# Kernel optimization log

Measured on AMD Instinct MI355X. Metric: run time of the kernel, lower is better.

The kernel has to match this reference:

```python
import jax, jax.numpy as jnp
import numpy as np
from jax.scipy.linalg import cho_solve

B, T, N, L, R, H, S = 32, 256, 256, 64, 16, 256, 8


def mT(A):
    return jnp.swapaxes(A, -1, -2)


def bmv(A, x):
    return jnp.einsum('...ij,...j->...i', A, x)


def bip(x, y):
    return jnp.sum(x * y, axis=-1)


def chol_bmv_solve(chol, v):
    return cho_solve((chol, True), v[..., None])[..., 0]


def setup_inputs():
    key = jax.random.key(0)
    ks = jax.random.split(key, 8)
    y = 3.0 * jax.random.uniform(ks[0], (B, T, N), dtype=jnp.float32)  # nonneg 'counts'
    eps = jax.random.normal(ks[1], (S, B, T, L), dtype=jnp.float32)    # reparam noise
    W1 = jax.random.normal(ks[2], (N, H), dtype=jnp.float32) / np.float32(np.sqrt(N))
    b1 = jnp.zeros((H,), jnp.float32)
    W2 = 0.05 * jax.random.normal(ks[3], (H, L + L * R), dtype=jnp.float32)
    b2 = jnp.zeros((L + L * R,), jnp.float32)
    F = 0.9 * jnp.linalg.qr(jax.random.normal(ks[4], (L, L), dtype=jnp.float32))[0]  # stable dynamics
    log_Q = jnp.full((L,), -1.0, jnp.float32)
    log_Q_0 = jnp.zeros((L,), jnp.float32)
    m_0 = 0.1 * jax.random.normal(ks[5], (L,), dtype=jnp.float32)
    C = jax.random.normal(ks[6], (N, L), dtype=jnp.float32) / np.float32(np.sqrt(L))
    b_read = jnp.full((N,), -1.0, jnp.float32)
    return dict(y=y, eps=eps, W1=W1, b1=b1, W2=W2, b2=b2, F=F, log_Q=log_Q,
                log_Q_0=log_Q_0, m_0=m_0, C=C, b_read=b_read, n_samples=S)


def _kf_update(m_p, P_p, k_t, J_t):
    # information-form measurement update: J_f = P_p^{-1} + J_t
    I = jnp.eye(P_p.shape[-1], dtype=P_p.dtype)
    Pp_chol = jnp.linalg.cholesky(P_p)
    h_p = chol_bmv_solve(Pp_chol, m_p)
    J_p = cho_solve((Pp_chol, True), jnp.broadcast_to(I, P_p.shape))
    J_f = J_p + J_t
    Jf_chol = jnp.linalg.cholesky(0.5 * (J_f + mT(J_f)))
    P_f = cho_solve((Jf_chol, True), jnp.broadcast_to(I, J_f.shape))
    P_f = 0.5 * (P_f + mT(P_f))
    m_f = chol_bmv_solve(Jf_chol, h_p + k_t)
    return m_f, P_f


def kalman_information_filter(k, J, F, Q_diag, m_0, Q_0_diag):
    Bb, Tt, Ll = k.shape
    m_p0 = jnp.broadcast_to(m_0, (Bb, Ll))
    P_p0 = jnp.broadcast_to(jnp.diag(Q_0_diag), (Bb, Ll, Ll))
    m_f0, P_f0 = _kf_update(m_p0, P_p0, k[:, 0], J[:, 0])
    Qd = jnp.diag(Q_diag)

    def step(carry, inp):
        m_prev, P_prev = carry
        k_t, J_t = inp
        m_p = m_prev @ F.T
        P_p = F @ P_prev @ F.T + Qd
        m_f, P_f = _kf_update(m_p, P_p, k_t, J_t)
        return (m_f, P_f), (m_f, P_f, m_p, P_p)

    inp = (jnp.swapaxes(k[:, 1:], 0, 1), jnp.swapaxes(J[:, 1:], 0, 1))
    _, (m_f_r, P_f_r, m_p_r, P_p_r) = jax.lax.scan(step, (m_f0, P_f0), inp)
    cat = lambda x0, xr: jnp.concatenate([x0[:, None], jnp.swapaxes(xr, 0, 1)], axis=1)
    return cat(m_f0, m_f_r), cat(P_f0, P_f_r), cat(m_p0, m_p_r), cat(P_p0, P_p_r)


def rts_smoother(m_p, P_p, m_f, P_f, F):
    def step(carry, inp):
        m_s_n, P_s_n = carry
        m_f_t, P_f_t, m_p_n, P_p_n = inp
        Pp_chol = jnp.linalg.cholesky(P_p_n)
        G = mT(cho_solve((Pp_chol, True), F @ P_f_t))  # G = P_f F^T P_p^{-1}
        m_s = m_f_t + bmv(G, m_s_n - m_p_n)
        P_s = P_f_t + G @ (P_s_n - P_p_n) @ mT(G)
        P_s = 0.5 * (P_s + mT(P_s))
        return (m_s, P_s), (m_s, P_s)

    inp = (jnp.swapaxes(m_f[:, :-1], 0, 1), jnp.swapaxes(P_f[:, :-1], 0, 1),
           jnp.swapaxes(m_p[:, 1:], 0, 1), jnp.swapaxes(P_p[:, 1:], 0, 1))
    _, (m_s_r, P_s_r) = jax.lax.scan(step, (m_f[:, -1], P_f[:, -1]), inp, reverse=True)
    m = jnp.concatenate([jnp.swapaxes(m_s_r, 0, 1), m_f[:, -1:]], axis=1)
    P = jnp.concatenate([jnp.swapaxes(P_s_r, 0, 1), P_f[:, -1:]], axis=1)
    return m, P


def alt_kl_step_0(m_s, m_f, m_0, P_s, Q_0_diag, a, A):
    P_sA = P_s @ A
    P_pA = A * Q_0_diag[:, None]
    AmTP_sA = mT(A) @ P_sA
    AmTP_pA = mT(A) @ P_pA
    AmTm_s = bmv(mT(A), m_s)
    AmTm_f = bmv(mT(A), m_f)
    P_p_inv_m_f = m_f / Q_0_diag
    P_p_inv_m_p = m_0 / Q_0_diag
    Ir = jnp.eye(A.shape[-1], dtype=A.dtype)
    logdet_triple = jnp.linalg.slogdet(Ir + AmTP_pA)[1]
    inner_p = bip(a, m_s) - 0.5 * bip(AmTm_s, AmTm_s) - 0.5 * jnp.trace(AmTP_sA, axis1=-2, axis2=-1)
    delta_logZ = 0.5 * (bip(m_f, P_p_inv_m_f) - bip(m_0, P_p_inv_m_p) + bip(AmTm_f, AmTm_f) - logdet_triple)
    return inner_p - delta_logZ


def alt_kl_step_t(m_s, m_f, m_p, P_s, P_p, a, A):
    P_sA = P_s @ A
    P_pA = P_p @ A
    P_p_chol = jnp.linalg.cholesky(P_p)
    AmTP_sA = mT(A) @ P_sA
    AmTP_pA = mT(A) @ P_pA
    AmTm_s = bmv(mT(A), m_s)
    AmTm_f = bmv(mT(A), m_f)
    P_p_inv_m_f = chol_bmv_solve(P_p_chol, m_f)
    P_p_inv_m_p = chol_bmv_solve(P_p_chol, m_p)
    Ir = jnp.eye(A.shape[-1], dtype=A.dtype)
    logdet_triple = jnp.linalg.slogdet(Ir + AmTP_pA)[1]
    inner_p = bip(a, m_s) - 0.5 * bip(AmTm_s, AmTm_s) - 0.5 * jnp.trace(AmTP_sA, axis1=-2, axis2=-1)
    delta_logZ = 0.5 * (bip(m_f, P_p_inv_m_f) - bip(m_p, P_p_inv_m_p) + bip(AmTm_f, AmTm_f) - logdet_triple)
    return inner_p - delta_logZ


def _forward(y, eps, W1, b1, W2, b2, F, log_Q, log_Q_0, m_0, C, b_read):
    # local encoder (all masks are identity since p_mask_* = 0)
    h = jnp.tanh(y @ W1 + b1)
    out = h @ W2 + b2
    k_y = out[..., :L]                                   # [B,T,L]
    K_y = out[..., L:].reshape(y.shape[0], y.shape[1], L, R)  # [B,T,L,R]
    Q_diag = jax.nn.softplus(log_Q)
    Q_0_diag = jax.nn.softplus(log_Q_0)
    m_f, P_f, m_p, P_p = kalman_information_filter(k_y, K_y @ mT(K_y), F, Q_diag, m_0, Q_0_diag)
    m, P = rts_smoother(m_p, P_p, m_f, P_f, F)
    kl_1 = alt_kl_step_0(m[:, 0], m_f[:, 0], m_0, P[:, 0], Q_0_diag, k_y[:, 0], K_y[:, 0])
    kl_t = alt_kl_step_t(m[:, 1:], m_f[:, 1:], m_p[:, 1:], P[:, 1:], P_p[:, 1:], k_y[:, 1:], K_y[:, 1:])
    kl = jnp.concatenate([kl_1[:, None], kl_t], axis=1)  # [B,T]
    P_chol = jnp.linalg.cholesky(P + 1e-5 * jnp.eye(L, dtype=P.dtype))
    z_s = m + bmv(P_chol, eps)                            # [S,B,T,L]
    log_rate = jnp.einsum('sbtl,nl->sbtn', z_s, C) + b_read
    ell = jnp.sum(y * log_rate - jnp.exp(log_rate), axis=-1).mean(axis=0)  # [B,T]
    return jnp.mean(jnp.sum(kl - ell, axis=-1))


def reference(y, eps, W1, b1, W2, b2, F, log_Q, log_Q_0, m_0, C, b_read, n_samples):
    return _forward(y, eps, W1, b1, W2, b2, F, log_Q, log_Q_0, m_0, C, b_read)
```

## Files before the change

kernel.cpp:

```cpp
#include <hip/hip_runtime.h>
#include <math.h>

#define B_ 32
#define T_ 256
#define N_ 256
#define L_ 64
#define R_ 16
#define H_ 256
#define NS_ 8
#define SEG 32
#define NSEG 8
#define ST 65
#define STM 67
#define STF 68
#define SBF 72
#define SU 20
#define PKN 2080
#define PIDX(i,j) ((((i)*((i)+1))>>1) + (j))

using f32x4  = __attribute__((ext_vector_type(4))) float;
using bf16x8 = __attribute__((ext_vector_type(8))) short;
using s16x4  = __attribute__((ext_vector_type(4))) short;

__device__ __forceinline__ float softplus_f(float x) { return log1pf(expf(x)); }
// ... 20 lines not shown
{ return __uint_as_float(((unsigned)(unsigned short)s)<<16); }

template<int SB>
__device__ __forceinline__ void mfma_mm64(const short* Ah, const short* Al,
                                          const short* Bh, const short* Bl,
                                          int w, int l, f32x4 acc[4])
{
  const int lr = l & 15, lg = l >> 4;
  const int arow = (w*16+lr)*SB;
#pragma unroll
  for (int ks = 0; ks < 2; ++ks) {
    const int ko = ks*32 + lg*8;
    bf16x8 ah = *(const bf16x8*)&Ah[arow + ko];
    bf16x8 al = *(const bf16x8*)&Al[arow + ko];
#pragma unroll
    for (int ct = 0; ct < 4; ++ct) {
      bf16x8 bh = *(const bf16x8*)&Bh[(ct*16+lr)*SB + ko];
      bf16x8 bl = *(const bf16x8*)&Bl[(ct*16+lr)*SB + ko];
      acc[ct] = __builtin_amdgcn_mfma_f32_16x16x32_bf16(ah, bh, acc[ct], 0,0,0);
      acc[ct] = __builtin_amdgcn_mfma_f32_16x16x32_bf16(ah, bl, acc[ct], 0,0,0);
      acc[ct] = __builtin_amdgcn_mfma_f32_16x16x32_bf16(al, bh, acc[ct], 0,0,0);
    }
  }
}

template<int SA>
__device__ __forceinline__ void chol64_blk(float* A, float* rdiag, float* dg, int tid)
{
#pragma unroll
  for (int kb = 0; kb < 4; ++kb) {
    const int o = kb*16;
    if (tid < 16) {
      const int ln = tid;
      float s[16];
#pragma unroll
      for (int j = 0; j < 16; ++j) s[j] = A[(o+ln)*SA + o + j];
#pragma unroll
      for (int k = 0; k < 16; ++k) {
        const float dk = fmaxf(__shfl(s[k], k, 64), 1e-30f);
        const float d = sqrtf(dk);
        const float rd = 1.f/d;
        const float lik = s[k]*rd;
        if (ln == k) { rdiag[o+k] = rd; if (dg) dg[o+k] = d; }
#pragma unroll
        for (int j = 0; j < 16; ++j) {
          const float ljk = __shfl(lik, j, 64);
          if (j > k && j <= ln) s[j] -= lik*ljk;
        }
        if (ln > k) s[k] = lik;
        else if (ln == k) s[k] = dk;
      }
#pragma unroll
      for (int j = 0; j < 16; ++j) A[(o+ln)*SA + o + j] = s[j];
    }
    __syncthreads();
    const int nr = 48 - o;
    if (nr > 0) {
      if (tid < nr) {
        const int r = o + 16 + tid;
        float x[16];
#pragma unroll
        for (int q = 0; q < 16; ++q) x[q] = A[r*SA + o + q];
#pragma unroll
        for (int j = 0; j < 16; ++j) {
          x[j] *= rdiag[o+j];
#pragma unroll
          for (int i2 = j+1; i2 < 16; ++i2) x[i2] -= A[(o+i2)*SA + o + j] * x[j];
        }
#pragma unroll
        for (int q = 0; q < 16; ++q) A[r*SA + o + q] = x[q];
      }
      __syncthreads();
      const int tot = nr*nr;
      for (int idx = tid; idx < tot; idx += 256) {
        const int i = o + 16 + idx / nr, j = o + 16 + idx % nr;
        float acc = A[i*SA + j];
#pragma unroll
        for (int k = 0; k < 16; ++k) acc -= A[i*SA + o + k] * A[j*SA + o + k];
        A[i*SA + j] = acc;
      }
      __syncthreads();
    }
  }
}

__device__ __forceinline__ void fwd16(float* x, const float* sS, const float* sSd)
{
#pragma unroll
  for (int a = 0; a < 16; ++a) {
    x[a] *= sSd[a];
#pragma unroll
    for (int i = a+1; i < 16; ++i) x[i] -= sS[i*17+a]*x[a];
  }
}

template<bool TANH, bool SPLIT>
__global__ __launch_bounds__(256) void gemm_kernel(
    const float* __restrict__ A, const float* __restrict__ Bw,
    const float* __restrict__ bias, float* __restrict__ C1,
    float* __restrict__ C2, int M, int Nn, int Kk)
{
  __shared__ float As[16][65];
  __shared__ float Bs[16][64];
  const int bm = blockIdx.y * 64, bn = blockIdx.x * 64;
  const int tid = threadIdx.x;
  const int rg = tid >> 4, cg = tid & 15;
  float acc[4][4] = {{0.f}};
  for (int k0 = 0; k0 < Kk; k0 += 16) {
    {
      const int kk = tid & 15, r0 = tid >> 4;
#pragma unroll
      for (int rr = 0; rr < 4; ++rr)
        As[kk][r0 + 16*rr] = A[(size_t)(bm + r0 + 16*rr) * Kk + k0 + kk];
    }
    {
      const int cc = tid & 63, kk = tid >> 6;
#pragma unroll
      for (int kr = 0; kr < 4; ++kr)
        Bs[kk + 4*kr][cc] = Bw[(size_t)(k0 + kk + 4*kr) * Nn + bn + cc];
    }
    __syncthreads();
#pragma unroll
    for (int k = 0; k < 16; ++k) {
      float a[4], bb[4];
#pragma unroll
      for (int i = 0; i < 4; ++i) a[i] = As[k][rg*4+i];
#pragma unroll
      for (int j = 0; j < 4; ++j) bb[j] = Bs[k][cg*4+j];
#pragma unroll
      for (int i = 0; i < 4; ++i)
#pragma unroll
        for (int j = 0; j < 4; ++j) acc[i][j] += a[i]*bb[j];
    }
    __syncthreads();
  }
#pragma unroll
  for (int i = 0; i < 4; ++i) {
    const int row = bm + rg*4 + i;
#pragma unroll
    for (int j = 0; j < 4; ++j) {
      const int col = bn + cg*4 + j;
      float v = acc[i][j] + bias[col];
      if (TANH) v = tanhf(v);
      if (SPLIT) {
        if (col < 64) C1[(size_t)row*64 + col] = v;
        else          C2[(size_t)row*1024 + (col-64)] = v;
      } else {
        C1[(size_t)row*Nn + col] = v;
      }
    }
  }
}

__global__ __launch_bounds__(256, 1) void filter_kernel(
    const float* __restrict__ kyg, const float* __restrict__ Kxg,
    const float* __restrict__ Fg, const float* __restrict__ logQ,
    const float* __restrict__ logQ0, const float* __restrict__ m0g,
    float* __restrict__ mf_g, float* __restrict__ mp_g,
    float* __restrict__ Pf_g, float* __restrict__ dpart_g,
    float* __restrict__ mfT_g)
{
  __shared__ float sB[64*STF];
  __shared__ __align__(16) char sPool[18432];
  __shared__ short sFh[64*SBF], sFl[64*SBF];
  __shared__ float sS[16*17], sSd[16];
  __shared__ float sQ[64], sQ0[64], skv[64], smf[64], smp[64], sv[16], sw[16];
  __shared__ float sldv;
  __shared__ f32x4 sRed4[256];
  float* sRed = (float*)sRed4;
  short* sXh = (short*)sPool;
  short* sXl = (short*)(sPool + 9216);
  float* sU  = (float*)sPool;
  float* sK  = (float*)(sPool + 5120);

  const int b = blockIdx.x, tid = threadIdx.x;
  const int w = tid >> 6, l = tid & 63;

#pragma unroll
  for (int q = 0; q < 4; ++q) {
    const int idx = q*1024 + tid*4;
    const int row = idx>>6, col = idx&63;
    float4 v = *(const float4*)&Fg[idx];
    s16x4 h4, l4;
    splitbf4(v, h4, l4);
    *(s16x4*)&sFh[row*SBF+col] = h4;
    *(s16x4*)&sFl[row*SBF+col] = l4;
  }
  if (tid < 64) {
    sQ[tid]  = softplus_f(logQ[tid]);
    sQ0[tid] = softplus_f(logQ0[tid]);
    smf[tid] = m0g[tid];
  }
  __syncthreads();

  for (int t = 0; t < T_; ++t) {
    const size_t bt = (size_t)b*T_ + t;
    if (t == 0) {
      for (int i = tid; i < 4096; i += 256) {
        const int r = i>>6, c = i&63;
        sB[r*STF+c] = (r==c) ? sQ0[r] : 0.f;
      }
      const float4 kreg = ((const float4*)(Kxg + bt*1024))[tid];
      *(float4*)&sK[(tid>>2)*SU + (tid&3)*4] = kreg;
      if (tid < 64) { smp[tid] = smf[tid]; skv[tid] = kyg[bt*64 + tid]; mp_g[bt*64+tid] = smp[tid]; }
      __syncthreads();
    } else {
#pragma unroll
      for (int q = 0; q < 4; ++q) {
        const int idx = q*1024 + tid*4;
        const int row = idx>>6, col = idx&63;
        float4 v = *(const float4*)&sB[row*STF+col];
        s16x4 h4, l4;
        splitbf4(v, h4, l4);
        *(s16x4*)&sXh[row*SBF+col] = h4;
        *(s16x4*)&sXl[row*SBF+col] = l4;
      }
      __syncthreads();
      const float4 kreg = ((const float4*)(Kxg + bt*1024))[tid];
      float kvreg = 0.f;
      if (tid < 64) kvreg = kyg[bt*64 + tid];
      f32x4 acc[4];
#pragma unroll
      for (int ct = 0; ct < 4; ++ct) acc[ct] = (f32x4){0.f,0.f,0.f,0.f};
      mfma_mm64<SBF>(sFh, sFl, sXh, sXl, w, l, acc);
      {
        const int i = tid & 63, jb = tid >> 6;
        float s = 0.f;
#pragma unroll
        for (int hq = 0; hq < 2; ++hq) {
          bf16x8 fh = *(const bf16x8*)&sFh[i*SBF + jb*16 + hq*8];
          bf16x8 fl = *(const bf16x8*)&sFl[i*SBF + jb*16 + hq*8];
#pragma unroll
          for (int j = 0; j < 8; ++j)
            s += (bf2f(fh[j]) + bf2f(fl[j])) * smf[jb*16 + hq*8 + j];
        }
        sRed[tid] = s;
      }
      __syncthreads();
      {
        const int lr = l & 15, lg = l >> 4;
#pragma unroll
        for (int ct = 0; ct < 4; ++ct)
#pragma unroll
          for (int r = 0; r < 4; ++r) {
            short hh, ll;
            splitbf(acc[ct][r], hh, ll);
            const int row = w*16 + lg*4 + r, col = ct*16 + lr;
            sXh[row*SBF+col] = hh; sXl[row*SBF+col] = ll;
          }
      }
      if (tid < 64) {
        const float mpv = sRed[tid] + sRed[tid+64] + sRed[tid+128] + sRed[tid+192];
        smp[tid] = mpv; mp_g[bt*64+tid] = mpv;
      }
      __syncthreads();
#pragma unroll
      for (int ct = 0; ct < 4; ++ct) acc[ct] = (f32x4){0.f,0.f,0.f,0.f};
      mfma_mm64<SBF>(sXh, sXl, sFh, sFl, w, l, acc);
      __syncthreads();
      {
        const int lr = l & 15, lg = l >> 4;
#pragma unroll
        for (int ct = 0; ct < 4; ++ct)
#pragma unroll
          for (int r = 0; r < 4; ++r) {
            const int row = w*16 + lg*4 + r, col = ct*16 + lr;
            sB[row*STF+col] = acc[ct][r] + ((row==col) ? sQ[row] : 0.f);
          }
      }
      *(float4*)&sK[(tid>>2)*SU + (tid&3)*4] = kreg;
      if (tid < 64) skv[tid] = kvreg;
      __syncthreads();
    }
    {
      const int i = tid & 63, rq = tid >> 6;
      float4 u = {0.f,0.f,0.f,0.f};
      for (int jb = 0; jb < 16; ++jb) {
        const float4 p4 = *(const float4*)&sB[i*STF + jb*4];
#pragma unroll
        for (int dj = 0; dj < 4; ++dj) {
          const float4 k4 = *(const float4*)&sK[(jb*4+dj)*SU + rq*4];
          const float pv = (dj==0) ? p4.x : (dj==1) ? p4.y : (dj==2) ? p4.z : p4.w;
          u.x += pv*k4.x; u.y += pv*k4.y; u.z += pv*k4.z; u.w += pv*k4.w;
        }
      }
      *(float4*)&sU[i*SU + rq*4] = u;
    }
    __syncthreads();
    {
      const int ib = tid >> 6, r1 = (tid >> 2) & 15, r2b = tid & 3;
      float4 part = {0.f,0.f,0.f,0.f};
      for (int ii = 0; ii < 16; ++ii) {
        const int i = ib*16 + ii;
        const float kv = sK[i*SU + r1];
        const float4 u4 = *(const float4*)&sU[i*SU + r2b*4];
        part.x += kv*u4.x; part.y += kv*u4.y; part.z += kv*u4.z; part.w += kv*u4.w;
      }
      sRed4[tid] = (f32x4){part.x, part.y, part.z, part.w};
    }
    __syncthreads();
    if (tid < 64) {
      const int r1 = tid >> 2, r2b = tid & 3;
      f32x4 s4 = sRed4[tid];
      s4 += sRed4[tid+64]; s4 += sRed4[tid+128]; s4 += sRed4[tid+192];
#pragma unroll
      for (int dj = 0; dj < 4; ++dj)
        sS[r1*17 + r2b*4 + dj] = s4[dj] + ((r1 == r2b*4+dj) ? 1.f : 0.f);
    }
    __syncthreads();
    if (tid < 16) {
      const int ln = tid;
      float s[16];
#pragma unroll
      for (int j = 0; j < 16; ++j) s[j] = sS[ln*17+j];
      float pd = 1.f;
#pragma unroll
      for (int k = 0; k < 16; ++k) {
        const float dk = fmaxf(__shfl(s[k], k, 64), 1e-30f);
        const float d = sqrtf(dk);
        const float rd = 1.f/d;
        pd *= dk;
        const float lik = s[k]*rd;
        if (ln == k) sSd[k] = rd;
#pragma unroll
        for (int j = 0; j < 16; ++j) {
          const float ljk = __shfl(lik, j, 64);
          if (j > k && j <= ln) s[j] -= lik*ljk;
        }
        if (ln > k) s[k] = lik;
        else if (ln == k) s[k] = d;
      }
#pragma unroll
      for (int j = 0; j < 16; ++j) sS[ln*17+j] = s[j];
      if (ln == 0) sldv = logf(pd);
    } else if (tid >= 64 && tid < 80) {
      const int r = tid - 64;
      float a = 0.f;
      for (int i = 0; i < 64; ++i) a += sK[i*SU+r] * smp[i];
      sv[r] = a;
    }
    __syncthreads();
    if (tid < 64) {
      float x[16];
#pragma unroll
      for (int q = 0; q < 4; ++q) {
        const float4 u4 = *(const float4*)&sU[tid*SU + q*4];
        x[q*4+0]=u4.x; x[q*4+1]=u4.y; x[q*4+2]=u4.z; x[q*4+3]=u4.w;
      }
      fwd16(x, sS, sSd);
#pragma unroll
      for (int q = 0; q < 4; ++q) {
        float4 u4 = {x[q*4+0], x[q*4+1], x[q*4+2], x[q*4+3]};
        *(float4*)&sU[tid*SU + q*4] = u4;
      }
    } else if (tid == 64) {
      float x[16];
#pragma unroll
      for (int r = 0; r < 16; ++r) x[r] = sv[r];
      fwd16(x, sS, sSd);
#pragma unroll
      for (int r = 0; r < 16; ++r) sw[r] = x[r];
    }
    __syncthreads();
    {
      const int rg = tid >> 4, cg = tid & 15;
      float acc2[4][4] = {{0.f}};
#pragma unroll
      for (int rb = 0; rb < 4; ++rb) {
        float4 a4[4], b4[4];
#pragma unroll
        for (int i = 0; i < 4; ++i) a4[i] = *(const float4*)&sU[(rg*4+i)*SU + rb*4];
#pragma unroll
        for (int jj = 0; jj < 4; ++jj) b4[jj] = *(const float4*)&sU[(cg+16*jj)*SU + rb*4];
#pragma unroll
        for (int i = 0; i < 4; ++i)
#pragma unroll
          for (int jj = 0; jj < 4; ++jj)
            acc2[i][jj] += a4[i].x*b4[jj].x + a4[i].y*b4[jj].y
                         + a4[i].z*b4[jj].z + a4[i].w*b4[jj].w;
      }
#pragma unroll
      for (int i = 0; i < 4; ++i)
#pragma unroll
        for (int jj = 0; jj < 4; ++jj) {
          const int r = rg*4+i, c = cg+16*jj;
          sB[r*STF+c] -= acc2[i][jj];
        }
    }
    __syncthreads();
    {
      const int i = tid & 63, jb = tid >> 6;
      float s = 0.f;
#pragma unroll
      for (int q = 0; q < 4; ++q) {
        const float4 p4 = *(const float4*)&sB[i*STF + jb*16 + q*4];
        s += p4.x*skv[jb*16+q*4+0] + p4.y*skv[jb*16+q*4+1]
           + p4.z*skv[jb*16+q*4+2] + p4.w*skv[jb*16+q*4+3];
      }
      sRed[tid] = s;
    }
    for (int i2 = tid; i2 < 4096; i2 += 256)
      Pf_g[bt*4096+i2] = sB[(i2>>6)*STF+(i2&63)];
    __syncthreads();
    if (tid < 64) {
      float a = smp[tid];
#pragma unroll
      for (int q = 0; q < 4; ++q) {
        const float4 u4 = *(const float4*)&sU[tid*SU + q*4];
        a -= u4.x*sw[q*4+0] + u4.y*sw[q*4+1] + u4.z*sw[q*4+2] + u4.w*sw[q*4+3];
      }
      a += sRed[tid] + sRed[tid+64] + sRed[tid+128] + sRed[tid+192];
      smf[tid] = a;
      mf_g[bt*64+tid] = a;
      if (t == T_-1) mfT_g[b*64+tid] = a;
    }
    __syncthreads();
    if (tid < 16) {
      float a = 0.f;
      for (int i = 0; i < 64; ++i) a += sK[i*SU+tid]*smf[i];
      float aa = a*a;
      aa += __shfl_xor(aa, 1, 64);
      aa += __shfl_xor(aa, 2, 64);
      aa += __shfl_xor(aa, 4, 64);
      aa += __shfl_xor(aa, 8, 64);
      if (tid == 0) {
        float dp = aa - sldv;
        if (t == 0) {
          float d1 = 0.f, d2 = 0.f;
          for (int i = 0; i < 64; ++i) {
            d1 += smf[i]*smf[i]/sQ0[i];
            d2 += smp[i]*smp[i]/sQ0[i];
          }
          dp = 0.5f*(d1 - d2 + dp);
        }
        dpart_g[bt] = dp;
      }
    }
    __syncthreads();
  }
}

__global__ __launch_bounds__(256) void gains_kernel(
    const float* __restrict__ Fg, const float* __restrict__ logQ,
    const float* __restrict__ mf_g, const float* __restrict__ mp_g,
    float* __restrict__ PfG_g, float* __restrict__ Cpk,
    float* __restrict__ d_g, float* __restrict__ dpart_g)
{
  const int blk = blockIdx.x;
  const int b = blk / (T_-1);
  const int n = 1 + (blk % (T_-1));
  const size_t btn = (size_t)b*T_ + n;
  const size_t btm = btn - 1;
  const int tid = threadIdx.x;
  const int rg = tid >> 4, cg = tid & 15;
  __shared__ float sA[64*ST];
  __shared__ float sM[64*STM];
  __shared__ float sPp[64*ST];
  __shared__ float sDi[64], sQd[64];
  __shared__ float smf1[64], smp[64];
  __shared__ float sd1d2[2];

  for (int i = tid; i < 4096; i += 256) sA[(i>>6)*ST + (i&63)] = PfG_g[btm*4096+i];
  if (tid < 64) {
    sM[tid*STM+64] = mf_g[btn*64+tid];
    sM[tid*STM+65] = mp_g[btn*64+tid];
    smf1[tid] = mf_g[btm*64+tid];
    smp[tid]  = mp_g[btn*64+tid];
    sQd[tid]  = softplus_f(logQ[tid]);
  }
  __syncthreads();
  {
    float acc[4][4] = {{0.f}};
#pragma unroll 4
    for (int k = 0; k < 64; ++k) {
      float a[4], bb[4];
#pragma unroll
      for (int i = 0; i < 4; ++i) a[i] = Fg[(rg*4+i)*64 + k];
#pragma unroll
      for (int j = 0; j < 4; ++j) bb[j] = sA[k*ST + cg*4+j];
#pragma unroll
      for (int i = 0; i < 4; ++i)
#pragma unroll
        for (int j = 0; j < 4; ++j) acc[i][j] += a[i]*bb[j];
    }
#pragma unroll
    for (int i = 0; i < 4; ++i)
#pragma unroll
      for (int j = 0; j < 4; ++j) sM[(rg*4+i)*STM + cg*4+j] = acc[i][j];
  }
  __syncthreads();
  {
    float acc[4][4] = {{0.f}};
#pragma unroll 4
    for (int k = 0; k < 64; ++k) {
      float a[4], bb[4];
#pragma unroll
      for (int i = 0; i < 4; ++i) a[i] = sM[(rg*4+i)*STM + k];
#pragma unroll
      for (int j = 0; j < 4; ++j) bb[j] = Fg[(cg*4+j)*64 + k];
#pragma unroll
      for (int i = 0; i < 4; ++i)
#pragma unroll
        for (int j = 0; j < 4; ++j) acc[i][j] += a[i]*bb[j];
    }
#pragma unroll
    for (int i = 0; i < 4; ++i)
#pragma unroll
      for (int j = 0; j < 4; ++j) {
        const int r = rg*4+i, c = cg*4+j;
        sPp[r*ST+c] = acc[i][j] + ((r==c) ? sQd[r] : 0.f);
      }
  }
  __syncthreads();
  chol64_blk<ST>(sPp, sDi, (float*)nullptr, tid);
#pragma unroll
  for (int jb = 0; jb < 4; ++jb) {
    const int o = jb*16;
    if (tid < 66) {
      const int c = tid;
      float x[16];
#pragma unroll
      for (int q = 0; q < 16; ++q) x[q] = sM[(o+q)*STM + c];
#pragma unroll
      for (int j = 0; j < 16; ++j) {
        x[j] *= sDi[o+j];
#pragma unroll
        for (int i = j+1; i < 16; ++i) x[i] -= sPp[(o+i)*ST + o+j] * x[j];
      }
#pragma unroll
      for (int q = 0; q < 16; ++q) sM[(o+q)*STM + c] = x[q];
    }
    __syncthreads();
    const int nr = 48 - o;
    if (nr > 0) {
      for (int idx = tid; idx < nr*66; idx += 256) {
        const int r = o + 16 + idx/66, c = idx%66;
        float acc = sM[r*STM + c];
#pragma unroll
        for (int k = 0; k < 16; ++k) acc -= sPp[r*ST + o+k] * sM[(o+k)*STM + c];
        sM[r*STM + c] = acc;
      }
      __syncthreads();
    }
  }
  if (tid == 64 || tid == 65) {
    float a = 0.f;
    for (int i = 0; i < 64; ++i) { const float v = sM[i*STM+tid]; a += v*v; }
    sd1d2[tid-64] = a;
  }
  {
    float acc[4][4] = {{0.f}};
#pragma unroll 2
    for (int k = 0; k < 64; ++k) {
      float a[4], bb[4];
#pragma unroll
      for (int i = 0; i < 4; ++i) a[i] = sM[k*STM + rg*4+i];
#pragma unroll
      for (int j = 0; j < 4; ++j) bb[j] = sM[k*STM + cg*4+j];
#pragma unroll
      for (int i = 0; i < 4; ++i)
#pragma unroll
        for (int j = 0; j < 4; ++j) acc[i][j] += a[i]*bb[j];
    }
#pragma unroll
    for (int i = 0; i < 4; ++i)
#pragma unroll
      for (int j = 0; j < 4; ++j)
        sA[(rg*4+i)*ST + (cg*4+j)] -= acc[i][j];
  }
  __syncthreads();
  for (int idx = tid; idx < 4096; idx += 256) {
    const int i = idx>>6, j = idx&63;
// ... 434 lines not shown
  sy[tid]  = yg[bt*256+tid];
  sbr[tid] = brg[tid];
  for (int i = tid; i < NS_*64; i += 256) {
    const int s = i >> 6, j = i & 63;
    sE[i] = epsg[(((size_t)s*B_ + b)*T_ + t)*64 + j];
  }
  __syncthreads();
  {
    const int i = tid & 63, rq = tid >> 6;
    float u[4] = {0.f,0.f,0.f,0.f};
    for (int j = 0; j < 64; ++j) {
      const float p = sPs[i*ST+j];
#pragma unroll
      for (int r = 0; r < 4; ++r) u[r] += p * sK[j*17 + rq*4 + r];
    }
#pragma unroll
    for (int r = 0; r < 4; ++r) sPA[i*17 + rq*4 + r] = u[r];
  }
  __syncthreads();
  {
    const int i = tid & 63, rq = tid >> 6;
    float a = 0.f;
#pragma unroll
    for (int r = 0; r < 4; ++r) a += sK[i*17+rq*4+r]*sPA[i*17+rq*4+r];
    red[tid] = a;
  }
  if (tid < 16) {
    float a = 0.f;
    for (int i = 0; i < 64; ++i) a += sK[i*17+tid]*sms[i];
    sv[tid] = a;
  }
  __syncthreads();
  for (int s2 = 128; s2 > 0; s2 >>= 1) {
    if (tid < s2) red[tid] += red[tid+s2];
    __syncthreads();
  }
  float klv = 0.f;
  if (tid == 0) {
    const float tr = red[0];
    float ip1 = 0.f;
    for (int i = 0; i < 64; ++i) ip1 += skv[i]*sms[i];
    float s2s = 0.f;
#pragma unroll
    for (int r = 0; r < 16; ++r) s2s += sv[r]*sv[r];
    klv = (ip1 - 0.5f*s2s - 0.5f*tr) - dpart_g[bt];
  }
  if (tid < 64) sPs[tid*ST+tid] += 1e-5f;
  __syncthreads();
  chol64_blk<ST>(sPs, sDi, sDg, tid);
#pragma unroll
  for (int p = 0; p < 2; ++p) {
    const int s = (tid >> 6) + 4*p, ll = tid & 63;
    float a = sms[ll];
    for (int j = 0; j < ll; ++j) a += sPs[ll*ST+j]*sE[s*64+j];
    a += sDg[ll]*sE[s*64+ll];
    sZ[s*ST+ll] = a;
  }
  __syncthreads();
  float accel = 0.f;
  for (int nc = 0; nc < 4; ++nc) {
    for (int i = tid; i < 4096; i += 256) sC[(i>>6)*ST+(i&63)] = Cg[nc*4096+i];
    __syncthreads();
#pragma unroll
    for (int p = 0; p < 2; ++p) {
      const int idx = p*256 + tid;
      const int s = idx >> 6, rn = idx & 63;
      const int nn2 = nc*64 + rn;
      float lr = sbr[nn2];
      for (int ll = 0; ll < 64; ++ll) lr += sZ[s*ST+ll]*sC[rn*ST+ll];
      accel += sy[nn2]*lr - expf(lr);
    }
    __syncthreads();
  }
  red[tid] = accel;
  __syncthreads();
  for (int s2 = 128; s2 > 0; s2 >>= 1) {
    if (tid < s2) red[tid] += red[tid+s2];
    __syncthreads();
  }
  if (tid == 0) val_g[bt] = klv - red[0]*(1.0f/NS_);
}

__global__ __launch_bounds__(256) void reduce_kernel(const float* __restrict__ val,
                                                     float* __restrict__ out)
{
  __shared__ float red[256];
  float acc = 0.f;
  for (int i = threadIdx.x; i < B_*T_; i += 256) acc += val[i];
  red[threadIdx.x] = acc;
  __syncthreads();
  for (int s2 = 128; s2 > 0; s2 >>= 1) {
    if (threadIdx.x < s2) red[threadIdx.x] += red[threadIdx.x+s2];
    __syncthreads();
  }
  if (threadIdx.x == 0) out[0] = red[0] / (float)B_;
}

__global__ void diag_kernel(float* out, float v)
{
  if (threadIdx.x == 0) out[0] = v;
}

extern "C" void kernel_launch(void* const* d_in, const int* in_sizes, int n_in,
                              void* d_out, int out_size, void* d_ws, size_t ws_size,
                              hipStream_t stream)
{
  const float* y    = (const float*)d_in[0];
  const float* eps  = (const float*)d_in[1];
  const float* W1   = (const float*)d_in[2];
  const float* b1   = (const float*)d_in[3];
  const float* W2   = (const float*)d_in[4];
  const float* b2   = (const float*)d_in[5];
  const float* F    = (const float*)d_in[6];
  const float* logQ = (const float*)d_in[7];
  const float* logQ0= (const float*)d_in[8];
  const float* m0   = (const float*)d_in[9];
  const float* C    = (const float*)d_in[10];
  const float* br   = (const float*)d_in[11];
  (void)in_sizes; (void)n_in; (void)out_size;

  char* ws = (char*)d_ws;
  float* out = (float*)d_out;

  auto al = [](size_t x){ return (x + 255) & ~(size_t)255; };
  size_t o = 0;
  float* ky    = (float*)(ws + o); o = al(o + (size_t)B_*T_*64*4);
  float* mf    = (float*)(ws + o); o = al(o + (size_t)B_*T_*64*4);
  float* mp    = (float*)(ws + o); o = al(o + (size_t)B_*T_*64*4);
  float* msb   = (float*)(ws + o); o = al(o + (size_t)B_*T_*64*4);
  float* dv    = (float*)(ws + o); o = al(o + (size_t)B_*T_*64*4);
  float* dpart = (float*)(ws + o); o = al(o + (size_t)B_*T_*4);
  float* val   = (float*)(ws + o); o = al(o + (size_t)B_*T_*4);
  float* Kx    = (float*)(ws + o); o = al(o + (size_t)B_*T_*1024*4);
  float* A1    = (float*)(ws + o); o = al(o + (size_t)B_*T_*4096*4);
  float* Cpk   = (float*)(ws + o); o = al(o + (size_t)B_*T_*PKN*4);
  float* Gseg  = (float*)(ws + o); o = al(o + (size_t)B_*NSEG*4096*4);
  float* cseg  = (float*)(ws + o); o = al(o + (size_t)B_*NSEG*PKN*4);
  float* dseg  = (float*)(ws + o); o = al(o + (size_t)B_*NSEG*64*4);
  float* InP   = (float*)(ws + o); o = al(o + (size_t)B_*NSEG*PKN*4);
  float* Inm   = (float*)(ws + o); o = al(o + (size_t)B_*NSEG*64*4);
  float* mfT   = (float*)(ws + o); o = al(o + (size_t)B_*64*4);
  float* h     = A1;

  if (ws_size < o) {
    diag_kernel<<<1, 64, 0, stream>>>(out, (float)((double)ws_size / 1048576.0));
    return;
  }

  dim3 blk(256);
  gemm_kernel<true,false><<<dim3(H_/64, (B_*T_)/64), blk, 0, stream>>>(
      y, W1, b1, h, (float*)nullptr, B_*T_, H_, N_);
  gemm_kernel<false,true><<<dim3((L_+L_*R_)/64, (B_*T_)/64), blk, 0, stream>>>(
      h, W2, b2, ky, Kx, B_*T_, L_+L_*R_, H_);
  filter_kernel<<<B_, blk, 0, stream>>>(ky, Kx, F, logQ, logQ0, m0,
                                        mf, mp, A1, dpart, mfT);
  gains_kernel<<<B_*(T_-1), blk, 0, stream>>>(F, logQ, mf, mp, A1, Cpk, dv, dpart);
  compose_kernel<<<B_*NSEG, blk, 65536 + 8320 + 1024 + 256 + 64, stream>>>(
      A1, Cpk, dv, Gseg, cseg, dseg);
  boundary_kernel<<<B_, blk, 0, stream>>>(A1, mfT, Gseg, cseg, dseg, InP, Inm);
  expand_kernel<<<B_*NSEG, blk, 0, stream>>>(A1, Cpk, dv, InP, Inm, msb);
  klell_kernel<<<B_*T_, blk, 0, stream>>>(y, eps, ky, Kx, C, br, Cpk, msb, dpart, val);
  reduce_kernel<<<1, blk, 0, stream>>>(val, (float*)d_out);
}
```

Baseline: 5.301 ms.

## Move filter low-rank update GEMMs to split-bf16 MFMA and fuse Pf epilogue

The per-timestep low-rank pieces of the sequential filter kernel now run on bf16x3 split MFMA instructions instead of scalar FP32 loops. These are the U=P·K product, the K^T·U Schur matrix and the V·V^T downdate. The kernel keeps split hi/lo copies of P, K^T, U^T and V in dynamic LDS. It fuses the Pf global store, the P·k reduction and the re-split of P into the downdate epilogue, which removes a separate conversion pass and several barriers per step. The cost is larger LDS use (about 90KB of dynamic shared memory) and a small loss of precision from the 3-term bf16 split.

```diff
diff --git a/kernel.cpp b/kernel.cpp
--- a/kernel.cpp
+++ b/kernel.cpp
@@ -196,6 +196,7 @@
   }
 }
 
+#define FLDS 90688
 __global__ __launch_bounds__(256, 1) void filter_kernel(
     const float* __restrict__ kyg, const float* __restrict__ Kxg,
     const float* __restrict__ Fg, const float* __restrict__ logQ,
@@ -204,21 +205,34 @@
     float* __restrict__ Pf_g, float* __restrict__ dpart_g,
     float* __restrict__ mfT_g)
 {
-  __shared__ float sB[64*STF];
-  __shared__ __align__(16) char sPool[18432];
-  __shared__ short sFh[64*SBF], sFl[64*SBF];
-  __shared__ float sS[16*17], sSd[16];
-  __shared__ float sQ[64], sQ0[64], skv[64], smf[64], smp[64], sv[16], sw[16];
+  extern __shared__ __align__(16) char fsm[];
+  float* sB  = (float*)fsm;
+  short* sFh = (short*)(fsm + 17408);
+  short* sFl = sFh + 64*SBF;
+  short* sXh = sFl + 64*SBF;
+  short* sXl = sXh + 64*SBF;
+  short* sVh = sXl + 64*SBF;
+  short* sVl = sVh + 64*SBF;
+  short* sKTh = sVl + 64*SBF;
+  short* sKTl = sKTh + 16*SBF;
+  short* sUTh = sKTl + 16*SBF;
+  short* sUTl = sUTh + 16*SBF;
+  float* sU  = (float*)(fsm + 81920);
+  float* sS  = (float*)(fsm + 87040);
+  float* sSd = (float*)(fsm + 88192);
+  float* sQ  = (float*)(fsm + 88256);
+  float* sQ0 = sQ + 64;
+  float* skv = sQ0 + 64;
+  float* smf = skv + 64;
+  float* smp = smf + 64;
+  float* sv  = smp + 64;
+  float* sw  = sv + 16;
+  float* sRed = (float*)(fsm + 89664);
   __shared__ float sldv;
-  __shared__ f32x4 sRed4[256];
-  float* sRed = (float*)sRed4;
-  short* sXh = (short*)sPool;
-  short* sXl = (short*)(sPool + 9216);
-  float* sU  = (float*)sPool;
-  float* sK  = (float*)(sPool + 5120);
 
   const int b = blockIdx.x, tid = threadIdx.x;
   const int w = tid >> 6, l = tid & 63;
+  const int lr = l & 15, lg = l >> 4;
 
 #pragma unroll
   for (int q = 0; q < 4; ++q) {
@@ -230,6 +244,10 @@
     *(s16x4*)&sFh[row*SBF+col] = h4;
     *(s16x4*)&sFl[row*SBF+col] = l4;
   }
+  for (int i = tid; i < 1024; i += 256) {
+    const int r = i>>4, c = 16 + (i&15);
+    sVh[r*SBF+c] = 0; sVl[r*SBF+c] = 0;
+  }
   if (tid < 64) {
     sQ[tid]  = softplus_f(logQ[tid]);
     sQ0[tid] = softplus_f(logQ0[tid]);
@@ -242,24 +260,27 @@
     if (t == 0) {
       for (int i = tid; i < 4096; i += 256) {
         const int r = i>>6, c = i&63;
-        sB[r*STF+c] = (r==c) ? sQ0[r] : 0.f;
-      }
-      const float4 kreg = ((const float4*)(Kxg + bt*1024))[tid];
-      *(float4*)&sK[(tid>>2)*SU + (tid&3)*4] = kreg;
-      if (tid < 64) { smp[tid] = smf[tid]; skv[tid] = kyg[bt*64 + tid]; mp_g[bt*64+tid] = smp[tid]; }
+        const float v = (r==c) ? sQ0[r] : 0.f;
+        sB[r*STF+c] = v;
+        short h, lo; splitbf(v, h, lo);
+        sXh[r*SBF+c] = h; sXl[r*SBF+c] = lo;
+      }
+      {
+        const float4 kreg = ((const float4*)(Kxg + bt*1024))[tid];
+        const int row = tid>>2, c0 = (tid&3)*4;
+        short h, lo;
+        splitbf(kreg.x,h,lo); sKTh[(c0+0)*SBF+row]=h; sKTl[(c0+0)*SBF+row]=lo;
+        splitbf(kreg.y,h,lo); sKTh[(c0+1)*SBF+row]=h; sKTl[(c0+1)*SBF+row]=lo;
+        splitbf(kreg.z,h,lo); sKTh[(c0+2)*SBF+row]=h; sKTl[(c0+2)*SBF+row]=lo;
+        splitbf(kreg.w,h,lo); sKTh[(c0+3)*SBF+row]=h; sKTl[(c0+3)*SBF+row]=lo;
+      }
+      if (tid < 64) {
+        smp[tid] = smf[tid];
+        skv[tid] = kyg[bt*64 + tid];
+        mp_g[bt*64+tid] = smp[tid];
+      }
       __syncthreads();
     } else {
-#pragma unroll
-      for (int q = 0; q < 4; ++q) {
-        const int idx = q*1024 + tid*4;
-        const int row = idx>>6, col = idx&63;
-        float4 v = *(const float4*)&sB[row*STF+col];
-        s16x4 h4, l4;
-        splitbf4(v, h4, l4);
-        *(s16x4*)&sXh[row*SBF+col] = h4;
-        *(s16x4*)&sXl[row*SBF+col] = l4;
-      }
-      __syncthreads();
       const float4 kreg = ((const float4*)(Kxg + bt*1024))[tid];
       float kvreg = 0.f;
       if (tid < 64) kvreg = kyg[bt*64 + tid];
@@ -281,18 +302,15 @@
         sRed[tid] = s;
       }
       __syncthreads();
-      {
-        const int lr = l & 15, lg = l >> 4;
-#pragma unroll
-        for (int ct = 0; ct < 4; ++ct)
-#pragma unroll
-          for (int r = 0; r < 4; ++r) {
-            short hh, ll;
-            splitbf(acc[ct][r], hh, ll);
-            const int row = w*16 + lg*4 + r, col = ct*16 + lr;
-            sXh[row*SBF+col] = hh; sXl[row*SBF+col] = ll;
-          }
-      }
+#pragma unroll
+      for (int ct = 0; ct < 4; ++ct)
+#pragma unroll
+        for (int r = 0; r < 4; ++r) {
+          short hh, ll;
+          splitbf(acc[ct][r], hh, ll);
+          const int row = w*16 + lg*4 + r, col = ct*16 + lr;
+          sXh[row*SBF+col] = hh; sXl[row*SBF+col] = ll;
+        }
       if (tid < 64) {
         const float mpv = sRed[tid] + sRed[tid+64] + sRed[tid+128] + sRed[tid+192];
         smp[tid] = mpv; mp_g[bt*64+tid] = mpv;
@@ -302,54 +320,74 @@
       for (int ct = 0; ct < 4; ++ct) acc[ct] = (f32x4){0.f,0.f,0.f,0.f};
       mfma_mm64<SBF>(sXh, sXl, sFh, sFl, w, l, acc);
       __syncthreads();
+#pragma unroll
+      for (int ct = 0; ct < 4; ++ct)
+#pragma unroll
+        for (int r = 0; r < 4; ++r) {
+          const int row = w*16 + lg*4 + r, col = ct*16 + lr;
+          const float pv = acc[ct][r] + ((row==col) ? sQ[row] : 0.f);
+          sB[row*STF+col] = pv;
+          short hh, ll; splitbf(pv, hh, ll);
+          sXh[row*SBF+col] = hh; sXl[row*SBF+col] = ll;
+        }
       {
-        const int lr = l & 15, lg = l >> 4;
-#pragma unroll
-        for (int ct = 0; ct < 4; ++ct)
-#pragma unroll
-          for (int r = 0; r < 4; ++r) {
-            const int row = w*16 + lg*4 + r, col = ct*16 + lr;
-            sB[row*STF+col] = acc[ct][r] + ((row==col) ? sQ[row] : 0.f);
-          }
-      }
-      *(float4*)&sK[(tid>>2)*SU + (tid&3)*4] = kreg;
+        const int row = tid>>2, c0 = (tid&3)*4;
+        short h, lo;
+        splitbf(kreg.x,h,lo); sKTh[(c0+0)*SBF+row]=h; sKTl[(c0+0)*SBF+row]=lo;
+        splitbf(kreg.y,h,lo); sKTh[(c0+1)*SBF+row]=h; sKTl[(c0+1)*SBF+row]=lo;
+        splitbf(kreg.z,h,lo); sKTh[(c0+2)*SBF+row]=h; sKTl[(c0+2)*SBF+row]=lo;
+        splitbf(kreg.w,h,lo); sKTh[(c0+3)*SBF+row]=h; sKTl[(c0+3)*SBF+row]=lo;
+      }
       if (tid < 64) skv[tid] = kvreg;
       __syncthreads();
     }
     {
-      const int i = tid & 63, rq = tid >> 6;
-      float4 u = {0.f,0.f,0.f,0.f};
-      for (int jb = 0; jb < 16; ++jb) {
-        const float4 p4 = *(const float4*)&sB[i*STF + jb*4];
-#pragma unroll
-        for (int dj = 0; dj < 4; ++dj) {
-          const float4 k4 = *(const float4*)&sK[(jb*4+dj)*SU + rq*4];
-          const float pv = (dj==0) ? p4.x : (dj==1) ? p4.y : (dj==2) ? p4.z : p4.w;
-          u.x += pv*k4.x; u.y += pv*k4.y; u.z += pv*k4.z; u.w += pv*k4.w;
-        }
-      }
-      *(float4*)&sU[i*SU + rq*4] = u;
-    }
-    __syncthreads();
-    {
-      const int ib = tid >> 6, r1 = (tid >> 2) & 15, r2b = tid & 3;
-      float4 part = {0.f,0.f,0.f,0.f};
-      for (int ii = 0; ii < 16; ++ii) {
-        const int i = ib*16 + ii;
-        const float kv = sK[i*SU + r1];
-        const float4 u4 = *(const float4*)&sU[i*SU + r2b*4];
-        part.x += kv*u4.x; part.y += kv*u4.y; part.z += kv*u4.z; part.w += kv*u4.w;
-      }
-      sRed4[tid] = (f32x4){part.x, part.y, part.z, part.w};
-    }
-    __syncthreads();
-    if (tid < 64) {
-      const int r1 = tid >> 2, r2b = tid & 3;
-      f32x4 s4 = sRed4[tid];
-      s4 += sRed4[tid+64]; s4 += sRed4[tid+128]; s4 += sRed4[tid+192];
-#pragma unroll
-      for (int dj = 0; dj < 4; ++dj)
-        sS[r1*17 + r2b*4 + dj] = s4[dj] + ((r1 == r2b*4+dj) ? 1.f : 0.f);
+      f32x4 u = (f32x4){0.f,0.f,0.f,0.f};
+      const int arow = (w*16+lr)*SBF;
+#pragma unroll
+      for (int ks = 0; ks < 2; ++ks) {
+        const int ko = ks*32 + lg*8;
+        bf16x8 ah = *(const bf16x8*)&sXh[arow + ko];
+        bf16x8 al = *(const bf16x8*)&sXl[arow + ko];
+        bf16x8 bh = *(const bf16x8*)&sKTh[lr*SBF + ko];
+        bf16x8 bl = *(const bf16x8*)&sKTl[lr*SBF + ko];
+        u = __builtin_amdgcn_mfma_f32_16x16x32_bf16(ah, bh, u, 0,0,0);
+        u = __builtin_amdgcn_mfma_f32_16x16x32_bf16(ah, bl, u, 0,0,0);
+        u = __builtin_amdgcn_mfma_f32_16x16x32_bf16(al, bh, u, 0,0,0);
+      }
+#pragma unroll
+      for (int r = 0; r < 4; ++r) {
+        const int row = w*16 + lg*4 + r;
+        sU[row*SU + lr] = u[r];
+        short hh, ll; splitbf(u[r], hh, ll);
+        sUTh[lr*SBF + row] = hh; sUTl[lr*SBF + row] = ll;
+      }
+    }
+    __syncthreads();
+    if (w == 0) {
+      f32x4 sa = (f32x4){0.f,0.f,0.f,0.f};
+#pragma unroll
+      for (int ks = 0; ks < 2; ++ks) {
+        const int ko = ks*32 + lg*8;
+        bf16x8 ah = *(const bf16x8*)&sKTh[lr*SBF + ko];
+        bf16x8 al = *(const bf16x8*)&sKTl[lr*SBF + ko];
+        bf16x8 bh = *(const bf16x8*)&sUTh[lr*SBF + ko];
+        bf16x8 bl = *(const bf16x8*)&sUTl[lr*SBF + ko];
+        sa = __builtin_amdgcn_mfma_f32_16x16x32_bf16(ah, bh, sa, 0,0,0);
+        sa = __builtin_amdgcn_mfma_f32_16x16x32_bf16(ah, bl, sa, 0,0,0);
+        sa = __builtin_amdgcn_mfma_f32_16x16x32_bf16(al, bh, sa, 0,0,0);
+      }
+#pragma unroll
+      for (int r = 0; r < 4; ++r) {
+        const int rs = lg*4 + r;
+        sS[rs*17 + lr] = sa[r] + ((rs == lr) ? 1.f : 0.f);
+      }
+    } else if (tid >= 64 && tid < 80) {
+      const int r = tid - 64;
+      float a = 0.f;
+      for (int i = 0; i < 64; ++i)
+        a += (bf2f(sKTh[r*SBF+i]) + bf2f(sKTl[r*SBF+i])) * smp[i];
+      sv[r] = a;
     }
     __syncthreads();
     if (tid < 16) {
@@ -377,11 +415,6 @@
 #pragma unroll
       for (int j = 0; j < 16; ++j) sS[ln*17+j] = s[j];
       if (ln == 0) sldv = logf(pd);
-    } else if (tid >= 64 && tid < 80) {
-      const int r = tid - 64;
-      float a = 0.f;
-      for (int i = 0; i < 64; ++i) a += sK[i*SU+r] * smp[i];
-      sv[r] = a;
     }
     __syncthreads();
     if (tid < 64) {
@@ -397,6 +430,11 @@
         float4 u4 = {x[q*4+0], x[q*4+1], x[q*4+2], x[q*4+3]};
         *(float4*)&sU[tid*SU + q*4] = u4;
       }
+#pragma unroll
+      for (int q = 0; q < 16; ++q) {
+        short hh, ll; splitbf(x[q], hh, ll);
+        sVh[tid*SBF + q] = hh; sVl[tid*SBF + q] = ll;
+      }
     } else if (tid == 64) {
       float x[16];
 #pragma unroll
@@ -407,44 +445,42 @@
     }
     __syncthreads();
     {
-      const int rg = tid >> 4, cg = tid & 15;
-      float acc2[4][4] = {{0.f}};
-#pragma unroll
-      for (int rb = 0; rb < 4; ++rb) {
-        float4 a4[4], b4[4];
-#pragma unroll
-        for (int i = 0; i < 4; ++i) a4[i] = *(const float4*)&sU[(rg*4+i)*SU + rb*4];
-#pragma unroll
-        for (int jj = 0; jj < 4; ++jj) b4[jj] = *(const float4*)&sU[(cg+16*jj)*SU + rb*4];
-#pragma unroll
-        for (int i = 0; i < 4; ++i)
-#pragma unroll
-          for (int jj = 0; jj < 4; ++jj)
-            acc2[i][jj] += a4[i].x*b4[jj].x + a4[i].y*b4[jj].y
-                         + a4[i].z*b4[jj].z + a4[i].w*b4[jj].w;
-      }
-#pragma unroll
-      for (int i = 0; i < 4; ++i)
-#pragma unroll
-        for (int jj = 0; jj < 4; ++jj) {
-          const int r = rg*4+i, c = cg+16*jj;
-          sB[r*STF+c] -= acc2[i][jj];
+      f32x4 acc2[4];
+#pragma unroll
+      for (int ct = 0; ct < 4; ++ct) acc2[ct] = (f32x4){0.f,0.f,0.f,0.f};
+      const int arow = (w*16+lr)*SBF;
+      const int ko = lg*8;
+      bf16x8 ah = *(const bf16x8*)&sVh[arow + ko];
+      bf16x8 al = *(const bf16x8*)&sVl[arow + ko];
+#pragma unroll
+      for (int ct = 0; ct < 4; ++ct) {
+        bf16x8 bh = *(const bf16x8*)&sVh[(ct*16+lr)*SBF + ko];
+        bf16x8 bl = *(const bf16x8*)&sVl[(ct*16+lr)*SBF + ko];
+        acc2[ct] = __builtin_amdgcn_mfma_f32_16x16x32_bf16(ah, bh, acc2[ct], 0,0,0);
+        acc2[ct] = __builtin_amdgcn_mfma_f32_16x16x32_bf16(ah, bl, acc2[ct], 0,0,0);
+        acc2[ct] = __builtin_amdgcn_mfma_f32_16x16x32_bf16(al, bh, acc2[ct], 0,0,0);
+      }
+      float pk[4] = {0.f,0.f,0.f,0.f};
+#pragma unroll
+      for (int ct = 0; ct < 4; ++ct)
+#pragma unroll
+        for (int r = 0; r < 4; ++r) {
+          const int row = w*16 + lg*4 + r, col = ct*16 + lr;
+          const float pf = sB[row*STF+col] - acc2[ct][r];
+          sB[row*STF+col] = pf;
+          short hh, ll; splitbf(pf, hh, ll);
+          sXh[row*SBF+col] = hh; sXl[row*SBF+col] = ll;
+          Pf_g[bt*4096 + row*64 + col] = pf;
+          pk[r] += pf * skv[col];
         }
-    }
-    __syncthreads();
-    {
-      const int i = tid & 63, jb = tid >> 6;
-      float s = 0.f;
-#pragma unroll
-      for (int q = 0; q < 4; ++q) {
-        const float4 p4 = *(const float4*)&sB[i*STF + jb*16 + q*4];
-        s += p4.x*skv[jb*16+q*4+0] + p4.y*skv[jb*16+q*4+1]
-           + p4.z*skv[jb*16+q*4+2] + p4.w*skv[jb*16+q*4+3];
-      }
-      sRed[tid] = s;
-    }
-    for (int i2 = tid; i2 < 4096; i2 += 256)
-      Pf_g[bt*4096+i2] = sB[(i2>>6)*STF+(i2&63)];
+#pragma unroll
+      for (int m = 1; m < 16; m <<= 1)
+#pragma unroll
+        for (int r = 0; r < 4; ++r) pk[r] += __shfl_xor(pk[r], m, 64);
+      if (lr == 0)
+#pragma unroll
+        for (int r = 0; r < 4; ++r) sRed[w*16 + lg*4 + r] = pk[r];
+    }
     __syncthreads();
     if (tid < 64) {
       float a = smp[tid];
@@ -453,7 +489,7 @@
         const float4 u4 = *(const float4*)&sU[tid*SU + q*4];
         a -= u4.x*sw[q*4+0] + u4.y*sw[q*4+1] + u4.z*sw[q*4+2] + u4.w*sw[q*4+3];
       }
-      a += sRed[tid] + sRed[tid+64] + sRed[tid+128] + sRed[tid+192];
+      a += sRed[tid];
       smf[tid] = a;
       mf_g[bt*64+tid] = a;
       if (t == T_-1) mfT_g[b*64+tid] = a;
@@ -461,7 +497,8 @@
     __syncthreads();
     if (tid < 16) {
       float a = 0.f;
-      for (int i = 0; i < 64; ++i) a += sK[i*SU+tid]*smf[i];
+      for (int i = 0; i < 64; ++i)
+        a += (bf2f(sKTh[tid*SBF+i]) + bf2f(sKTl[tid*SBF+i])) * smf[i];
       float aa = a*a;
       aa += __shfl_xor(aa, 1, 64);
       aa += __shfl_xor(aa, 2, 64);
@@ -1202,8 +1239,8 @@
       y, W1, b1, h, (float*)nullptr, B_*T_, H_, N_);
   gemm_kernel<false,true><<<dim3((L_+L_*R_)/64, (B_*T_)/64), blk, 0, stream>>>(
       h, W2, b2, ky, Kx, B_*T_, L_+L_*R_, H_);
-  filter_kernel<<<B_, blk, 0, stream>>>(ky, Kx, F, logQ, logQ0, m0,
-                                        mf, mp, A1, dpart, mfT);
+  filter_kernel<<<B_, blk, FLDS, stream>>>(ky, Kx, F, logQ, logQ0, m0,
+                                           mf, mp, A1, dpart, mfT);
   gains_kernel<<<B_*(T_-1), blk, 0, stream>>>(F, logQ, mf, mp, A1, Cpk, dv, dpart);
   compose_kernel<<<B_*NSEG, blk, 65536 + 8320 + 1024 + 256 + 64, stream>>>(
       A1, Cpk, dv, Gseg, cseg, dseg);
```

New measurement: 5.508 ms. +3.9%, slower.
